# Kernel tuning notes

Measured on AMD Instinct MI355X. Metric: run time of the kernel, lower is better.

Reference implementation:

```python
import jax, jax.numpy as jnp
import numpy as np

N_ATOMS = 40000
N_EDGES = 640000
N_BASIS = 128    # n_atom_basis == n_filters
N_RBF = 20
N_LAYERS = 3
MAX_Z = 100
CUTOFF = 5.0


def _ssp(x):
    # shifted softplus: softplus(x) - log(2)
    return jax.nn.softplus(x) - jnp.log(2.0).astype(x.dtype)


def setup_inputs() -> dict:
    key = jax.random.key(0)
    ks = jax.random.split(key, 16)
    s = 0.05
    inp = {
        'atomic_numbers': jax.random.randint(ks[0], (N_ATOMS,), 0, MAX_Z),
        'r_ij': jax.random.normal(ks[1], (N_EDGES, 3), dtype=jnp.float32),
        'idx_i': jnp.sort(jax.random.randint(ks[2], (N_EDGES,), 0, N_ATOMS)),
        'idx_j': jax.random.randint(ks[3], (N_EDGES,), 0, N_ATOMS),
        # learned parameters (stacked over interaction blocks)
        'emb': jax.random.normal(ks[4], (MAX_Z, N_BASIS), dtype=jnp.float32) * s,
        'in2f_W': jax.random.normal(ks[5], (N_LAYERS, N_BASIS, N_BASIS), dtype=jnp.float32) * s,
        'filt_W1': jax.random.normal(ks[6], (N_LAYERS, N_RBF, N_BASIS), dtype=jnp.float32) * s,
        'filt_b1': jax.random.normal(ks[7], (N_LAYERS, N_BASIS), dtype=jnp.float32) * s,
        'filt_W2': jax.random.normal(ks[8], (N_LAYERS, N_BASIS, N_BASIS), dtype=jnp.float32) * s,
        'filt_b2': jax.random.normal(ks[9], (N_LAYERS, N_BASIS), dtype=jnp.float32) * s,
        'out_W1': jax.random.normal(ks[10], (N_LAYERS, N_BASIS, N_BASIS), dtype=jnp.float32) * s,
        'out_b1': jax.random.normal(ks[11], (N_LAYERS, N_BASIS), dtype=jnp.float32) * s,
        'out_W2': jax.random.normal(ks[12], (N_LAYERS, N_BASIS, N_BASIS), dtype=jnp.float32) * s,
        'out_b2': jax.random.normal(ks[13], (N_LAYERS, N_BASIS), dtype=jnp.float32) * s,
    }
    return inp


def reference(atomic_numbers, r_ij, idx_i, idx_j, emb, in2f_W,
              filt_W1, filt_b1, filt_W2, filt_b2,
              out_W1, out_b1, out_W2, out_b2):
    x = emb[atomic_numbers]                                   # [N, F]
    # pairwise distances and radial basis expansion (GaussianRBF)
    d_ij = jnp.linalg.norm(r_ij, axis=1)                      # [E]
    offsets = jnp.linspace(0.0, CUTOFF, N_RBF, dtype=d_ij.dtype)
    coeff = -0.5 / (offsets[1] - offsets[0]) ** 2
    f_ij = jnp.exp(coeff * (d_ij[:, None] - offsets[None, :]) ** 2)  # [E, n_rbf]
    # cosine cutoff
    rcut_ij = 0.5 * (jnp.cos(d_ij * jnp.pi / CUTOFF) + 1.0) * (d_ij < CUTOFF)
    for l in range(N_LAYERS):
        h = x @ in2f_W[l]                                     # in2f (no bias) [N, F]
        Wij = _ssp(f_ij @ filt_W1[l] + filt_b1[l]) @ filt_W2[l] + filt_b2[l]
        Wij = Wij * rcut_ij[:, None]                          # [E, F]
        msg = h[idx_j] * Wij                                  # gather + filter-multiply
        agg = jax.ops.segment_sum(msg, idx_i, num_segments=N_ATOMS)  # scatter-sum [N, F]
        v = _ssp(agg @ out_W1[l] + out_b1[l]) @ out_W2[l] + out_b2[l]
        x = x + v                                             # residual update
    return x
```

## Files before the change

### kernel.cpp

```cpp
#include <hip/hip_runtime.h>
#include <math.h>

#define N_ATOMS 40000
#define N_EDGES 640000
#define NB      128
#define NRBF    20
#define NLAYERS 3
#define CUTOFF  5.0f
#define DELTA   (CUTOFF / 19.0f)
#define RBF_COEFF (-0.5f / (DELTA * DELTA))
#define LN2F    0.69314718055994531f

#define KTAB    4096
#define TSCALE  ((float)KTAB / CUTOFF)
#define EPB     256
#define EBLKS   (N_EDGES / EPB)
#define TABBLKS 2049

typedef __attribute__((ext_vector_type(8))) short bf16x8;
typedef __attribute__((ext_vector_type(4))) short bf16x4;
typedef __attribute__((ext_vector_type(4))) float fx4;

__device__ __forceinline__ float ssp_f(float x) {
    return fmaxf(x, 0.f) + __logf(1.f + __expf(-fabsf(x))) - LN2F;
}

__device__ __forceinline__ unsigned short bf16_rne(float x) {
    unsigned u = __float_as_uint(x);
    unsigned r = u + 0x7fffu + ((u >> 16) & 1u);
    return (unsigned short)(r >> 16);
}

__device__ __forceinline__ float bfl(unsigned u) { return __uint_as_float(u << 16); }
__device__ __forceinline__ float bfh(unsigned u) { return __uint_as_float(u & 0xffff0000u); }


template<int ZERO>
__device__ __forceinline__ void stage_A_agg(float* __restrict__ A, int row0, int kc,
                                            short* Ah, int tid) {
    #pragma unroll
    for (int it = 0; it < 4; ++it) {
        int idx4 = tid + it * 256;
        int r = idx4 >> 4, kq = (idx4 & 15) << 2;
        float* src = A + (size_t)(row0 + r) * NB + kc * 64 + kq;
        float4 v = *(const float4*)src;
        if (ZERO) *(float4*)src = make_float4(0.f, 0.f, 0.f, 0.f);
        bf16x4 hs;
        const float* vf = (const float*)&v;
        #pragma unroll
        for (int j = 0; j < 4; ++j) hs[j] = (short)bf16_rne(vf[j]);
        int wi = r * 64 + (kq ^ ((r & 7) << 3));
        *(bf16x4*)(Ah + wi) = hs;
    }
}

__device__ __forceinline__ void stage_A_emb(const float* __restrict__ emb,
                                            const int* __restrict__ z, int row0, int kc,
                                            short* Ah, int tid) {
    #pragma unroll
    for (int it = 0; it < 4; ++it) {
        int idx4 = tid + it * 256;
        int r = idx4 >> 4, kq = (idx4 & 15) << 2;
        int zr = z[row0 + r];
        float4 v = *(const float4*)(emb + (size_t)zr * NB + kc * 64 + kq);
        bf16x4 hs;
        const float* vf = (const float*)&v;
        #pragma unroll
        for (int j = 0; j < 4; ++j) hs[j] = (short)bf16_rne(vf[j]);
        int wi = r * 64 + (kq ^ ((r & 7) << 3));
        *(bf16x4*)(Ah + wi) = hs;
    }
}

__device__ __forceinline__ void stage_W(const short* __restrict__ imgh,
                                        short* Wh, int tid) {
    #pragma unroll
    for (int it = 0; it < 4; ++it) {
        int i = tid + it * 256;
        ((bf16x8*)Wh)[i] = ((const bf16x8*)imgh)[i];
    }
}

__device__ __forceinline__ void stage_W_f32(const float* __restrict__ W, int kc,
                                            short* Wh, int tid) {
    #pragma unroll
    for (int it = 0; it < 8; ++it) {
        int i = tid + it * 256;
        int kl = i >> 5;
        int c0 = (i & 31) << 2;
        float4 v = *(const float4*)(W + (size_t)(kc * 64 + kl) * NB + c0);
        const float* vf = (const float*)&v;
        #pragma unroll
        for (int j = 0; j < 4; ++j) {
            int col = c0 + j;
            Wh[col * 64 + (kl ^ ((col & 7) << 3))] = (short)bf16_rne(vf[j]);
        }
    }
}

__device__ __forceinline__ void g_compute(const short* AH, int choff,
                                          const short* Wh,
                                          int wr, int wc, int lane, fx4 acc[2][4]) {
    #pragma unroll
    for (int ks = 0; ks < 2; ++ks) {
        int kb = ks * 32 + (lane >> 4) * 8;
        bf16x8 a_h[2];
        #pragma unroll
        for (int s = 0; s < 2; ++s) {
            int r = wr + s * 16 + (lane & 15);
            int idx = choff + r * 64 + (kb ^ ((r & 7) << 3));
            a_h[s] = *(const bf16x8*)(AH + idx);
        }
        #pragma unroll
        for (int c = 0; c < 4; ++c) {
            int col = wc + c * 16 + (lane & 15);
            int idx = col * 64 + (kb ^ ((col & 7) << 3));
            bf16x8 b_h = *(const bf16x8*)(Wh + idx);
            #pragma unroll
            for (int s = 0; s < 2; ++s)
                acc[s][c] = __builtin_amdgcn_mfma_f32_16x16x32_bf16(a_h[s], b_h, acc[s][c], 0, 0, 0);
        }
    }
}

#define P0_GEMM 625
#define P0_ZERO 1250
#define P0_TAB  TABBLKS
#define P0_DST  625
#define P0_WPR  64
__global__ __launch_bounds__(256) void k_pre0(const int* __restrict__ z,
                                              const float* __restrict__ emb,
                                              const float* __restrict__ r_ij,
                                              const int* __restrict__ ii,
                                              const int* __restrict__ jj,
                                              const float* __restrict__ in2f,
                                              const float* __restrict__ oW1,
                                              const float* __restrict__ oW2,
                                              const float* __restrict__ fW1,
                                              const float* __restrict__ fb1,
                                              const float* __restrict__ fW2,
                                              const float* __restrict__ fb2,
                                              unsigned short* __restrict__ HB,
                                              unsigned short* __restrict__ TabB,
                                              float* __restrict__ AGG,
                                              uint2* __restrict__ PK,
                                              short* __restrict__ Wimg) {
    __shared__ short APOOL[12288];
    int bid = blockIdx.x, tid = threadIdx.x;

    if (bid < P0_GEMM) {
        short* Ah = APOOL;
        short* Wh = APOOL + 4096;
        int wave = tid >> 6, lane = tid & 63;
        int wr = (wave & 1) * 32, wc = (wave >> 1) * 64;
        int row0 = bid * 64;
        fx4 acc[2][4];
        #pragma unroll
        for (int s = 0; s < 2; ++s)
            #pragma unroll
            for (int c = 0; c < 4; ++c)
                acc[s][c] = (fx4){0.f, 0.f, 0.f, 0.f};
        for (int kc = 0; kc < 2; ++kc) {
            if (kc) __syncthreads();
            stage_A_emb(emb, z, row0, kc, Ah, tid);
            stage_W_f32(in2f, kc, Wh, tid);
            __syncthreads();
            g_compute(Ah, 0, Wh, wr, wc, lane, acc);
        }
        #pragma unroll
        for (int s = 0; s < 2; ++s)
            #pragma unroll
            for (int c = 0; c < 4; ++c) {
                int colg = wc + c * 16 + (lane & 15);
                #pragma unroll
                for (int reg = 0; reg < 4; ++reg) {
                    int rowg = row0 + wr + s * 16 + (lane >> 4) * 4 + reg;
                    HB[(size_t)rowg * NB + colg] = bf16_rne(acc[s][c][reg]);
                }
            }
    } else if (bid < P0_GEMM + P0_ZERO) {
        int base = (bid - P0_GEMM) * 4096 + tid * 16;
        float4 zv = make_float4(0.f, 0.f, 0.f, 0.f);
        float4* p = (float4*)(AGG + base);
        p[0] = zv; p[1] = zv; p[2] = zv; p[3] = zv;
    } else if (bid < P0_GEMM + P0_ZERO + P0_TAB) {
        int tb = bid - (P0_GEMM + P0_ZERO);
        int half = tid >> 7, f = tid & 127;
        int r = tb * 2 + half;
        float* tl = (float*)APOOL;
        float val = 0.f;
        float d = (float)r * (CUTOFF / (float)KTAB);
        if (r < KTAB) {
            float a = fb1[f];
            #pragma unroll
            for (int q = 0; q < NRBF; ++q) {
                float dr = d - (float)q * DELTA;
                a += __expf(RBF_COEFF * dr * dr) * fW1[q * NB + f];
            }
            tl[half * NB + f] = ssp_f(a);
        }
        __syncthreads();
        if (r < KTAB) {
            float w = fb2[f];
            #pragma unroll 4
            for (int k = 0; k < NB; ++k) w += tl[half * NB + k] * fW2[k * NB + f];
            float rc = 0.5f * (__cosf(d * ((float)M_PI / CUTOFF)) + 1.f);
            val = w * rc;
        }
        TabB[(size_t)r * NB + f] = bf16_rne(val);
    } else if (bid < P0_GEMM + P0_ZERO + P0_TAB + P0_DST) {
        int e = (bid - (P0_GEMM + P0_ZERO + P0_TAB)) * 1024 + tid * 4;
        const float4* rv = (const float4*)(r_ij + (size_t)e * 3);
        float4 a = rv[0], b = rv[1], c = rv[2];
        int4 iv = *(const int4*)(ii + e);
        int4 jv = *(const int4*)(jj + e);
        float d0 = sqrtf(a.x * a.x + a.y * a.y + a.z * a.z);
        float d1 = sqrtf(a.w * a.w + b.x * b.x + b.y * b.y);
        float d2 = sqrtf(b.z * b.z + b.w * b.w + c.x * c.x);
        float d3 = sqrtf(c.y * c.y + c.z * c.z + c.w * c.w);
        float u0 = fminf(d0 * TSCALE + 0.5f, (float)KTAB);
        float u1 = fminf(d1 * TSCALE + 0.5f, (float)KTAB);
        float u2 = fminf(d2 * TSCALE + 0.5f, (float)KTAB);
        float u3 = fminf(d3 * TSCALE + 0.5f, (float)KTAB);
        uint4 w0, w1;
        w0.x = __float_as_uint(u0); w0.y = ((unsigned)iv.x << 16) | (unsigned)jv.x;
        w0.z = __float_as_uint(u1); w0.w = ((unsigned)iv.y << 16) | (unsigned)jv.y;
        w1.x = __float_as_uint(u2); w1.y = ((unsigned)iv.z << 16) | (unsigned)jv.z;
        w1.z = __float_as_uint(u3); w1.w = ((unsigned)iv.w << 16) | (unsigned)jv.w;
        *(uint4*)(PK + e) = w0;
        *(uint4*)(PK + e + 2) = w1;
    } else {
        int b2 = bid - (P0_GEMM + P0_ZERO + P0_TAB + P0_DST);
        int w = 1 + (b2 >> 3), seg = b2 & 7;
        int layer = w / 3, which = w % 3;
        const float* W = (which == 0 ? in2f : which == 1 ? oW1 : oW2)
                         + (size_t)layer * NB * NB;
        short* hi = Wimg + (size_t)w * 16384;
        int i0 = seg * 2048;
        #pragma unroll
        for (int ofs = 0; ofs < 2048; ofs += 256) {
            int i = i0 + ofs + tid;
            int k = i >> 7, col = i & 127;
            int kc = k >> 6, kl = k & 63;
            hi[kc * 8192 + col * 64 + (kl ^ ((col & 7) << 3))] = (short)bf16_rne(W[i]);
        }
    }
}

__global__ __launch_bounds__(256) void k_edge(const uint2* __restrict__ PK,
                                              const unsigned* __restrict__ HBv,
                                              const unsigned* __restrict__ TabU,
                                              float* __restrict__ AGG,
                                              const float* __restrict__ nW1,
                                              const float* __restrict__ nb1,
                                              const float* __restrict__ nW2,
                                              const float* __restrict__ nb2,
                                              unsigned short* __restrict__ TabN) {
    __shared__ uint2 m_s[EPB];
    __shared__ float t_lds[256];
    int tid = threadIdx.x;
    int bid = blockIdx.x;

    if (bid >= EBLKS) {
        int tb = bid - EBLKS;
        int half = tid >> 7, f = tid & 127;
        int r = tb * 2 + half;
        float val = 0.f;
        float d = (float)r * (CUTOFF / (float)KTAB);
        if (r < KTAB) {
            float a = nb1[f];
            #pragma unroll
            for (int q = 0; q < NRBF; ++q) {
                float dr = d - (float)q * DELTA;
                a += __expf(RBF_COEFF * dr * dr) * nW1[q * NB + f];
            }
            t_lds[half * NB + f] = ssp_f(a);
        }
        __syncthreads();
        if (r < KTAB) {
            float w = nb2[f];
            #pragma unroll 4
            for (int k = 0; k < NB; ++k) w += t_lds[half * NB + k] * nW2[k * NB + f];
            float rc = 0.5f * (__cosf(d * ((float)M_PI / CUTOFF)) + 1.f);
            val = w * rc;
        }
        TabN[(size_t)r * NB + f] = bf16_rne(val);
        return;
    }

    int e0 = bid * EPB;
    m_s[tid] = PK[e0 + tid];
    __syncthreads();

    int wave = tid >> 6, lane = tid & 63;
    int wbase = wave << 6;

    float axA = 0.f, ayA = 0.f, axB = 0.f, ayB = 0.f;
    int curA = -1, curB = -1;
    int nfA = 0, nfB = 0;

    #pragma unroll 4
    for (int t = 0; t < 32; ++t) {
        uint2 mA = m_s[wbase + t];
        uint2 mB = m_s[wbase + 32 + t];

        int kA = (int)__uint_as_float(mA.x);
        int kB = (int)__uint_as_float(mB.x);
        int iaA = (int)(mA.y >> 16), jaA = (int)(mA.y & 0xffffu);
        int iaB = (int)(mB.y >> 16), jaB = (int)(mB.y & 0xffffu);

        unsigned tvA = TabU[kA * 64 + lane];
        unsigned tvB = TabU[kB * 64 + lane];
        unsigned hqA = HBv[jaA * 64 + lane];
        unsigned hqB = HBv[jaB * 64 + lane];

        if (iaA != curA) {
            if (curA >= 0) {
                float* p = AGG + curA * NB + 2 * lane;
                if (nfA == 0) { atomicAdd(p, axA); atomicAdd(p + 1, ayA); }
                else          { *(float2*)p = make_float2(axA, ayA); }
                ++nfA;
            }
            axA = 0.f; ayA = 0.f;
            curA = iaA;
        }
        axA = fmaf(bfl(hqA), bfl(tvA), axA);
        ayA = fmaf(bfh(hqA), bfh(tvA), ayA);

        if (iaB != curB) {
            if (curB >= 0) {
                float* p = AGG + curB * NB + 2 * lane;
                if (nfB == 0) { atomicAdd(p, axB); atomicAdd(p + 1, ayB); }
                else          { *(float2*)p = make_float2(axB, ayB); }
                ++nfB;
            }
            axB = 0.f; ayB = 0.f;
            curB = iaB;
        }
        axB = fmaf(bfl(hqB), bfl(tvB), axB);
        ayB = fmaf(bfh(hqB), bfh(tvB), ayB);
    }
    if (curA >= 0) {
        float* p = AGG + curA * NB + 2 * lane;
        atomicAdd(p, axA); atomicAdd(p + 1, ayA);
    }
    if (curB >= 0) {
        float* p = AGG + curB * NB + 2 * lane;
        atomicAdd(p, axB); atomicAdd(p + 1, ayB);
    }
}

template<int FIRST, int LAST>
__global__ __launch_bounds__(256) void k_fuse(float* __restrict__ AGG,
                                              const short* __restrict__ img1,
                                              const float* __restrict__ b1,
                                              const short* __restrict__ img2,
                                              const float* __restrict__ b2,
                                              const short* __restrict__ img0n,
                                              const int* __restrict__ z,
                                              const float* __restrict__ emb,
                                              float* __restrict__ X,
                                              unsigned short* __restrict__ HB) {
    __shared__ short POOL[16384];
    short* Ah = POOL;
    short* Th = POOL;
    short* Wh = POOL + 8192;

    int tid = threadIdx.x;
    int wave = tid >> 6, lane = tid & 63;
    int wr = (wave & 1) * 32, wc = (wave >> 1) * 64;
    int row0 = blockIdx.x * 64;

    fx4 accT[2][4];
    #pragma unroll
    for (int s = 0; s < 2; ++s)
        #pragma unroll
        for (int c = 0; c < 4; ++c)
            accT[s][c] = (fx4){0.f, 0.f, 0.f, 0.f};
    for (int kc = 0; kc < 2; ++kc) {
        if (kc) __syncthreads();
        stage_A_agg<!LAST>(AGG, row0, kc, Ah, tid);
        stage_W(img1 + kc * 8192, Wh, tid);
        __syncthreads();
        g_compute(Ah, 0, Wh, wr, wc, lane, accT);
    }
    __syncthreads();

    #pragma unroll
    for (int s = 0; s < 2; ++s)
        #pragma unroll
        for (int c = 0; c < 4; ++c) {
            int colg = wc + c * 16 + (lane & 15);
            float bv = b1[colg];
            int kc2 = colg >> 6, kl = colg & 63;
            #pragma unroll
            for (int reg = 0; reg < 4; ++reg) {
                int rl = wr + s * 16 + (lane >> 4) * 4 + reg;
                float t = ssp_f(accT[s][c][reg] + bv);
                Th[kc2 * 4096 + rl * 64 + (kl ^ ((rl & 7) << 3))] = (short)bf16_rne(t);
            }
        }
    stage_W(img2, Wh, tid);
    __syncthreads();

    fx4 accV[2][4];
    #pragma unroll
    for (int s = 0; s < 2; ++s)
        #pragma unroll
        for (int c = 0; c < 4; ++c)
            accV[s][c] = (fx4){0.f, 0.f, 0.f, 0.f};
    g_compute(Th, 0, Wh, wr, wc, lane, accV);
    __syncthreads();
    stage_W(img2 + 8192, Wh, tid);
    __syncthreads();
    g_compute(Th, 4096, Wh, wr, wc, lane, accV);
    __syncthreads();

    #pragma unroll
    for (int s = 0; s < 2; ++s)
        #pragma unroll
        for (int c = 0; c < 4; ++c) {
            int colg = wc + c * 16 + (lane & 15);
            float bv = b2[colg];
            int kc2 = colg >> 6, kl = colg & 63;
            #pragma unroll
            for (int reg = 0; reg < 4; ++reg) {
                int rowg = row0 + wr + s * 16 + (lane >> 4) * 4 + reg;
                size_t o = (size_t)rowg * NB + colg;
                float xo;
                if (FIRST) xo = emb[(size_t)z[rowg] * NB + colg];
                else       xo = X[o];
                float xn = xo + accV[s][c][reg] + bv;
                X[o] = xn;
                if (!LAST) {
                    int rl = wr + s * 16 + (lane >> 4) * 4 + reg;
                    Th[kc2 * 4096 + rl * 64 + (kl ^ ((rl & 7) << 3))] = (short)bf16_rne(xn);
                }
            }
        }
    if (LAST) return;

    stage_W(img0n, Wh, tid);
    __syncthreads();
    fx4 accH[2][4];
    #pragma unroll
    for (int s = 0; s < 2; ++s)
        #pragma unroll
        for (int c = 0; c < 4; ++c)
            accH[s][c] = (fx4){0.f, 0.f, 0.f, 0.f};
    g_compute(Th, 0, Wh, wr, wc, lane, accH);
    __syncthreads();
    stage_W(img0n + 8192, Wh, tid);
    __syncthreads();
    g_compute(Th, 4096, Wh, wr, wc, lane, accH);

    #pragma unroll
    for (int s = 0; s < 2; ++s)
        #pragma unroll
        for (int c = 0; c < 4; ++c) {
            int colg = wc + c * 16 + (lane & 15);
            #pragma unroll
            for (int reg = 0; reg < 4; ++reg) {
                int rowg = row0 + wr + s * 16 + (lane >> 4) * 4 + reg;
                HB[(size_t)rowg * NB + colg] = bf16_rne(accH[s][c][reg]);
            }
        }
}

extern "C" void kernel_launch(void* const* d_in, const int* in_sizes, int n_in,
                              void* d_out, int out_size, void* d_ws, size_t ws_size,
                              hipStream_t stream) {
    const int*   z    = (const int*)  d_in[0];
    const float* rij  = (const float*)d_in[1];
    const int*   ii   = (const int*)  d_in[2];
    const int*   jj   = (const int*)  d_in[3];
    const float* emb  = (const float*)d_in[4];
    const float* in2f = (const float*)d_in[5];
    const float* fW1  = (const float*)d_in[6];
    const float* fb1  = (const float*)d_in[7];
    const float* fW2  = (const float*)d_in[8];
    const float* fb2  = (const float*)d_in[9];
    const float* oW1  = (const float*)d_in[10];
    const float* ob1  = (const float*)d_in[11];
    const float* oW2  = (const float*)d_in[12];
    const float* ob2  = (const float*)d_in[13];

    const int NXF = N_ATOMS * NB;

    float* X = (float*)d_out;
    unsigned short* HB   = (unsigned short*)d_ws;
    float*          AGG  = (float*)(HB + (size_t)NXF);
    uint2*          PK   = (uint2*)(AGG + (size_t)NXF);
    unsigned short* Tab0 = (unsigned short*)(PK + N_EDGES);
    unsigned short* Tab1 = Tab0 + (size_t)4098 * NB;
    short*          Wimg = (short*)(Tab1 + (size_t)4098 * NB);

    k_pre0<<<P0_GEMM + P0_ZERO + P0_TAB + P0_DST + P0_WPR, 256, 0, stream>>>(
        z, emb, rij, ii, jj, in2f, oW1, oW2,
        fW1, fb1, fW2, fb2, HB, Tab0, AGG, PK, Wimg);

    for (int l = 0; l < NLAYERS; ++l) {
        unsigned short* TabCur = (l & 1) ? Tab1 : Tab0;
        unsigned short* TabNxt = (l & 1) ? Tab0 : Tab1;
        int ln = (l < NLAYERS - 1) ? l + 1 : 0;
        int grid_e = EBLKS + ((l < NLAYERS - 1) ? TABBLKS : 0);

        k_edge<<<grid_e, 256, 0, stream>>>(PK,
                                           (const unsigned*)HB,
                                           (const unsigned*)TabCur,
                                           AGG,
                                           fW1 + (size_t)ln * NRBF * NB,
                                           fb1 + (size_t)ln * NB,
                                           fW2 + (size_t)ln * NB * NB,
                                           fb2 + (size_t)ln * NB,
                                           TabNxt);

        const short* img1  = Wimg + (size_t)(l * 3 + 1) * 16384;
        const short* img2  = Wimg + (size_t)(l * 3 + 2) * 16384;
        const short* img0n = Wimg + (size_t)((l + 1 < NLAYERS ? (l + 1) * 3 : 3)) * 16384;

        if (l == 0)
            k_fuse<1, 0><<<N_ATOMS / 64, 256, 0, stream>>>(AGG, img1, ob1 + (size_t)l * NB,
                                                           img2, ob2 + (size_t)l * NB,
                                                           img0n, z, emb, X, HB);
        else if (l < NLAYERS - 1)
            k_fuse<0, 0><<<N_ATOMS / 64, 256, 0, stream>>>(AGG, img1, ob1 + (size_t)l * NB,
                                                           img2, ob2 + (size_t)l * NB,
                                                           img0n, z, emb, X, HB);
        else
            k_fuse<0, 1><<<N_ATOMS / 64, 256, 0, stream>>>(AGG, img1, ob1 + (size_t)l * NB,
                                                           img2, ob2 + (size_t)l * NB,
                                                           img0n, z, emb, X, HB);
    }
}
```

Baseline: 232.9 us.

## Shrink filter table to 128 rows in LDS with linear interpolation

Reduces the precomputed distance-indexed filter table from 4096 nearest-neighbour rows to 128 rows plus a guard row. Each edge block copies the table into shared memory and linearly interpolates between adjacent rows, replacing global table gathers with LDS reads. Edges per block double to 512 to amortise the table load, and the table-build blocks shrink accordingly. The cost is extra interpolation arithmetic and lower accuracy versus the finer table, along with fewer, larger edge blocks.

```diff
diff --git a/kernel.cpp b/kernel.cpp
--- a/kernel.cpp
+++ b/kernel.cpp
@@ -11,11 +11,12 @@
 #define RBF_COEFF (-0.5f / (DELTA * DELTA))
 #define LN2F    0.69314718055994531f
 
-#define KTAB    4096
+#define KTAB    128
+#define TROWS   (KTAB + 2)
 #define TSCALE  ((float)KTAB / CUTOFF)
-#define EPB     256
+#define EPB     512
 #define EBLKS   (N_EDGES / EPB)
-#define TABBLKS 2049
+#define TABBLKS 65
 
 typedef __attribute__((ext_vector_type(8))) short bf16x8;
 typedef __attribute__((ext_vector_type(4))) short bf16x4;
@@ -218,10 +219,10 @@
         float d1 = sqrtf(a.w * a.w + b.x * b.x + b.y * b.y);
         float d2 = sqrtf(b.z * b.z + b.w * b.w + c.x * c.x);
         float d3 = sqrtf(c.y * c.y + c.z * c.z + c.w * c.w);
-        float u0 = fminf(d0 * TSCALE + 0.5f, (float)KTAB);
-        float u1 = fminf(d1 * TSCALE + 0.5f, (float)KTAB);
-        float u2 = fminf(d2 * TSCALE + 0.5f, (float)KTAB);
-        float u3 = fminf(d3 * TSCALE + 0.5f, (float)KTAB);
+        float u0 = fminf(d0 * TSCALE, (float)KTAB);
+        float u1 = fminf(d1 * TSCALE, (float)KTAB);
+        float u2 = fminf(d2 * TSCALE, (float)KTAB);
+        float u3 = fminf(d3 * TSCALE, (float)KTAB);
         uint4 w0, w1;
         w0.x = __float_as_uint(u0); w0.y = ((unsigned)iv.x << 16) | (unsigned)jv.x;
         w0.z = __float_as_uint(u1); w0.w = ((unsigned)iv.y << 16) | (unsigned)jv.y;
@@ -249,15 +250,15 @@
 
 __global__ __launch_bounds__(256) void k_edge(const uint2* __restrict__ PK,
                                               const unsigned* __restrict__ HBv,
-                                              const unsigned* __restrict__ TabU,
+                                              const unsigned* __restrict__ TabG,
                                               float* __restrict__ AGG,
                                               const float* __restrict__ nW1,
                                               const float* __restrict__ nb1,
                                               const float* __restrict__ nW2,
                                               const float* __restrict__ nb2,
                                               unsigned short* __restrict__ TabN) {
+    __shared__ unsigned tab_s[TROWS * 64];
     __shared__ uint2 m_s[EPB];
-    __shared__ float t_lds[256];
     int tid = threadIdx.x;
     int bid = blockIdx.x;
 
@@ -265,6 +266,7 @@
         int tb = bid - EBLKS;
         int half = tid >> 7, f = tid & 127;
         int r = tb * 2 + half;
+        float* tl = (float*)tab_s;
         float val = 0.f;
         float d = (float)r * (CUTOFF / (float)KTAB);
         if (r < KTAB) {
@@ -274,13 +276,13 @@
                 float dr = d - (float)q * DELTA;
                 a += __expf(RBF_COEFF * dr * dr) * nW1[q * NB + f];
             }
-            t_lds[half * NB + f] = ssp_f(a);
+            tl[half * NB + f] = ssp_f(a);
         }
         __syncthreads();
         if (r < KTAB) {
             float w = nb2[f];
             #pragma unroll 4
-            for (int k = 0; k < NB; ++k) w += t_lds[half * NB + k] * nW2[k * NB + f];
+            for (int k = 0; k < NB; ++k) w += tl[half * NB + k] * nW2[k * NB + f];
             float rc = 0.5f * (__cosf(d * ((float)M_PI / CUTOFF)) + 1.f);
             val = w * rc;
         }
@@ -288,31 +290,44 @@
         return;
     }
 
+    for (int i = tid; i < TROWS * 32; i += 256)
+        ((uint2*)tab_s)[i] = ((const uint2*)TabG)[i];
     int e0 = bid * EPB;
-    m_s[tid] = PK[e0 + tid];
+    m_s[tid]       = PK[e0 + tid];
+    m_s[tid + 256] = PK[e0 + 256 + tid];
     __syncthreads();
 
     int wave = tid >> 6, lane = tid & 63;
-    int wbase = wave << 6;
+    int wbase = wave << 7;
 
     float axA = 0.f, ayA = 0.f, axB = 0.f, ayB = 0.f;
     int curA = -1, curB = -1;
     int nfA = 0, nfB = 0;
 
-    #pragma unroll 4
-    for (int t = 0; t < 32; ++t) {
+    #pragma unroll 2
+    for (int t = 0; t < 64; ++t) {
         uint2 mA = m_s[wbase + t];
-        uint2 mB = m_s[wbase + 32 + t];
-
-        int kA = (int)__uint_as_float(mA.x);
-        int kB = (int)__uint_as_float(mB.x);
+        uint2 mB = m_s[wbase + 64 + t];
+
+        float uA = __uint_as_float(mA.x);
+        float uB = __uint_as_float(mB.x);
+        int kA = (int)uA, kB = (int)uB;
+        float frA = uA - (float)kA;
+        float frB = uB - (float)kB;
         int iaA = (int)(mA.y >> 16), jaA = (int)(mA.y & 0xffffu);
         int iaB = (int)(mB.y >> 16), jaB = (int)(mB.y & 0xffffu);
 
-        unsigned tvA = TabU[kA * 64 + lane];
-        unsigned tvB = TabU[kB * 64 + lane];
+        unsigned t0A = tab_s[kA * 64 + lane];
+        unsigned t1A = tab_s[kA * 64 + 64 + lane];
+        unsigned t0B = tab_s[kB * 64 + lane];
+        unsigned t1B = tab_s[kB * 64 + 64 + lane];
         unsigned hqA = HBv[jaA * 64 + lane];
         unsigned hqB = HBv[jaB * 64 + lane];
+
+        float w0A = fmaf(frA, bfl(t1A) - bfl(t0A), bfl(t0A));
+        float w1A = fmaf(frA, bfh(t1A) - bfh(t0A), bfh(t0A));
+        float w0B = fmaf(frB, bfl(t1B) - bfl(t0B), bfl(t0B));
+        float w1B = fmaf(frB, bfh(t1B) - bfh(t0B), bfh(t0B));
 
         if (iaA != curA) {
             if (curA >= 0) {
@@ -324,8 +339,8 @@
             axA = 0.f; ayA = 0.f;
             curA = iaA;
         }
-        axA = fmaf(bfl(hqA), bfl(tvA), axA);
-        ayA = fmaf(bfh(hqA), bfh(tvA), ayA);
+        axA = fmaf(bfl(hqA), w0A, axA);
+        ayA = fmaf(bfh(hqA), w1A, ayA);
 
         if (iaB != curB) {
             if (curB >= 0) {
@@ -337,8 +352,8 @@
             axB = 0.f; ayB = 0.f;
             curB = iaB;
         }
-        axB = fmaf(bfl(hqB), bfl(tvB), axB);
-        ayB = fmaf(bfh(hqB), bfh(tvB), ayB);
+        axB = fmaf(bfl(hqB), w0B, axB);
+        ayB = fmaf(bfh(hqB), w1B, ayB);
     }
     if (curA >= 0) {
         float* p = AGG + curA * NB + 2 * lane;
@@ -492,8 +507,8 @@
     float*          AGG  = (float*)(HB + (size_t)NXF);
     uint2*          PK   = (uint2*)(AGG + (size_t)NXF);
     unsigned short* Tab0 = (unsigned short*)(PK + N_EDGES);
-    unsigned short* Tab1 = Tab0 + (size_t)4098 * NB;
-    short*          Wimg = (short*)(Tab1 + (size_t)4098 * NB);
+    unsigned short* Tab1 = Tab0 + (size_t)TROWS * NB;
+    short*          Wimg = (short*)(Tab1 + (size_t)TROWS * NB);
 
     k_pre0<<<P0_GEMM + P0_ZERO + P0_TAB + P0_DST + P0_WPR, 256, 0, stream>>>(
         z, emb, rij, ii, jj, in2f, oW1, oW2,
```

New measurement: 261.1 us. 12.1% more time.

## Use CSR row pointers for atom-owned segment sums and shrink filter table with interpolation

Applied to the files above, without the earlier changes.

Builds a CSR row-pointer array by binary search over the sorted idx_i, then assigns each wave a fixed range of atoms so segment sums are written with plain stores instead of atomics. This removes the separate AGG zeroing pass and per-layer re-zeroing, and atoms with no edges get explicit zero writes. The filter lookup table shrinks from 4096 to 256 rows and uses linear interpolation between adjacent rows, which costs an extra table load per edge but makes the table much cheaper to build and more cache-resident. Per-wave work now depends on atom degree, so load balance is less even than the fixed edge blocking it replaces.

```diff
diff --git a/kernel.cpp b/kernel.cpp
--- a/kernel.cpp
+++ b/kernel.cpp
@@ -11,11 +11,11 @@
 #define RBF_COEFF (-0.5f / (DELTA * DELTA))
 #define LN2F    0.69314718055994531f
 
-#define KTAB    4096
+#define KTAB    256
+#define TROWS   (KTAB + 2)
 #define TSCALE  ((float)KTAB / CUTOFF)
-#define EPB     256
-#define EBLKS   (N_EDGES / EPB)
-#define TABBLKS 2049
+#define EBLKS   1250
+#define TABBLKS (TROWS / 2)
 
 typedef __attribute__((ext_vector_type(8))) short bf16x8;
 typedef __attribute__((ext_vector_type(4))) short bf16x4;
@@ -35,16 +35,13 @@
 __device__ __forceinline__ float bfh(unsigned u) { return __uint_as_float(u & 0xffff0000u); }
 
 
-template<int ZERO>
-__device__ __forceinline__ void stage_A_agg(float* __restrict__ A, int row0, int kc,
+__device__ __forceinline__ void stage_A_f32(const float* __restrict__ A, int row0, int kc,
                                             short* Ah, int tid) {
     #pragma unroll
     for (int it = 0; it < 4; ++it) {
         int idx4 = tid + it * 256;
         int r = idx4 >> 4, kq = (idx4 & 15) << 2;
-        float* src = A + (size_t)(row0 + r) * NB + kc * 64 + kq;
-        float4 v = *(const float4*)src;
-        if (ZERO) *(float4*)src = make_float4(0.f, 0.f, 0.f, 0.f);
+        float4 v = *(const float4*)(A + (size_t)(row0 + r) * NB + kc * 64 + kq);
         bf16x4 hs;
         const float* vf = (const float*)&v;
         #pragma unroll
@@ -124,10 +121,10 @@
 }
 
 #define P0_GEMM 625
-#define P0_ZERO 1250
 #define P0_TAB  TABBLKS
 #define P0_DST  625
 #define P0_WPR  64
+#define P0_RPT  157
 __global__ __launch_bounds__(256) void k_pre0(const int* __restrict__ z,
                                               const float* __restrict__ emb,
                                               const float* __restrict__ r_ij,
@@ -142,8 +139,8 @@
                                               const float* __restrict__ fb2,
                                               unsigned short* __restrict__ HB,
                                               unsigned short* __restrict__ TabB,
-                                              float* __restrict__ AGG,
                                               uint2* __restrict__ PK,
+                                              int* __restrict__ rp,
                                               short* __restrict__ Wimg) {
     __shared__ short APOOL[12288];
     int bid = blockIdx.x, tid = threadIdx.x;
@@ -178,13 +175,8 @@
                     HB[(size_t)rowg * NB + colg] = bf16_rne(acc[s][c][reg]);
                 }
             }
-    } else if (bid < P0_GEMM + P0_ZERO) {
-        int base = (bid - P0_GEMM) * 4096 + tid * 16;
-        float4 zv = make_float4(0.f, 0.f, 0.f, 0.f);
-        float4* p = (float4*)(AGG + base);
-        p[0] = zv; p[1] = zv; p[2] = zv; p[3] = zv;
-    } else if (bid < P0_GEMM + P0_ZERO + P0_TAB) {
-        int tb = bid - (P0_GEMM + P0_ZERO);
+    } else if (bid < P0_GEMM + P0_TAB) {
+        int tb = bid - P0_GEMM;
         int half = tid >> 7, f = tid & 127;
         int r = tb * 2 + half;
         float* tl = (float*)APOOL;
@@ -208,8 +200,8 @@
             val = w * rc;
         }
         TabB[(size_t)r * NB + f] = bf16_rne(val);
-    } else if (bid < P0_GEMM + P0_ZERO + P0_TAB + P0_DST) {
-        int e = (bid - (P0_GEMM + P0_ZERO + P0_TAB)) * 1024 + tid * 4;
+    } else if (bid < P0_GEMM + P0_TAB + P0_DST) {
+        int e = (bid - (P0_GEMM + P0_TAB)) * 1024 + tid * 4;
         const float4* rv = (const float4*)(r_ij + (size_t)e * 3);
         float4 a = rv[0], b = rv[1], c = rv[2];
         int4 iv = *(const int4*)(ii + e);
@@ -218,10 +210,10 @@
         float d1 = sqrtf(a.w * a.w + b.x * b.x + b.y * b.y);
         float d2 = sqrtf(b.z * b.z + b.w * b.w + c.x * c.x);
         float d3 = sqrtf(c.y * c.y + c.z * c.z + c.w * c.w);
-        float u0 = fminf(d0 * TSCALE + 0.5f, (float)KTAB);
-        float u1 = fminf(d1 * TSCALE + 0.5f, (float)KTAB);
-        float u2 = fminf(d2 * TSCALE + 0.5f, (float)KTAB);
-        float u3 = fminf(d3 * TSCALE + 0.5f, (float)KTAB);
+        float u0 = fminf(d0 * TSCALE, (float)KTAB);
+        float u1 = fminf(d1 * TSCALE, (float)KTAB);
+        float u2 = fminf(d2 * TSCALE, (float)KTAB);
+        float u3 = fminf(d3 * TSCALE, (float)KTAB);
         uint4 w0, w1;
         w0.x = __float_as_uint(u0); w0.y = ((unsigned)iv.x << 16) | (unsigned)jv.x;
         w0.z = __float_as_uint(u1); w0.w = ((unsigned)iv.y << 16) | (unsigned)jv.y;
@@ -229,8 +221,8 @@
         w1.z = __float_as_uint(u3); w1.w = ((unsigned)iv.w << 16) | (unsigned)jv.w;
         *(uint4*)(PK + e) = w0;
         *(uint4*)(PK + e + 2) = w1;
-    } else {
-        int b2 = bid - (P0_GEMM + P0_ZERO + P0_TAB + P0_DST);
+    } else if (bid < P0_GEMM + P0_TAB + P0_DST + P0_WPR) {
+        int b2 = bid - (P0_GEMM + P0_TAB + P0_DST);
         int w = 1 + (b2 >> 3), seg = b2 & 7;
         int layer = w / 3, which = w % 3;
         const float* W = (which == 0 ? in2f : which == 1 ? oW1 : oW2)
@@ -244,10 +236,22 @@
             int kc = k >> 6, kl = k & 63;
             hi[kc * 8192 + col * 64 + (kl ^ ((col & 7) << 3))] = (short)bf16_rne(W[i]);
         }
-    }
-}
-
-__global__ __launch_bounds__(256) void k_edge(const uint2* __restrict__ PK,
+    } else {
+        int a = (bid - (P0_GEMM + P0_TAB + P0_DST + P0_WPR)) * 256 + tid;
+        if (a <= N_ATOMS) {
+            int lo = 0, hi = N_EDGES;
+            #pragma unroll 1
+            while (lo < hi) {
+                int mid = (lo + hi) >> 1;
+                if (ii[mid] < a) lo = mid + 1; else hi = mid;
+            }
+            rp[a] = lo;
+        }
+    }
+}
+
+__global__ __launch_bounds__(256) void k_edge(const int* __restrict__ rp,
+                                              const uint2* __restrict__ PK,
                                               const unsigned* __restrict__ HBv,
                                               const unsigned* __restrict__ TabU,
                                               float* __restrict__ AGG,
@@ -256,7 +260,6 @@
                                               const float* __restrict__ nW2,
                                               const float* __restrict__ nb2,
                                               unsigned short* __restrict__ TabN) {
-    __shared__ uint2 m_s[EPB];
     __shared__ float t_lds[256];
     int tid = threadIdx.x;
     int bid = blockIdx.x;
@@ -288,70 +291,79 @@
         return;
     }
 
-    int e0 = bid * EPB;
-    m_s[tid] = PK[e0 + tid];
-    __syncthreads();
-
     int wave = tid >> 6, lane = tid & 63;
-    int wbase = wave << 6;
+    int A0 = (bid * 4 + wave) * 8;
+    int esA = rp[A0],     eeA = rp[A0 + 4];
+    int esB = rp[A0 + 4], eeB = rp[A0 + 8];
 
     float axA = 0.f, ayA = 0.f, axB = 0.f, ayB = 0.f;
     int curA = -1, curB = -1;
-    int nfA = 0, nfB = 0;
-
-    #pragma unroll 4
-    for (int t = 0; t < 32; ++t) {
-        uint2 mA = m_s[wbase + t];
-        uint2 mB = m_s[wbase + 32 + t];
-
-        int kA = (int)__uint_as_float(mA.x);
-        int kB = (int)__uint_as_float(mB.x);
-        int iaA = (int)(mA.y >> 16), jaA = (int)(mA.y & 0xffffu);
-        int iaB = (int)(mB.y >> 16), jaB = (int)(mB.y & 0xffffu);
-
-        unsigned tvA = TabU[kA * 64 + lane];
-        unsigned tvB = TabU[kB * 64 + lane];
-        unsigned hqA = HBv[jaA * 64 + lane];
-        unsigned hqB = HBv[jaB * 64 + lane];
-
-        if (iaA != curA) {
-            if (curA >= 0) {
-                float* p = AGG + curA * NB + 2 * lane;
-                if (nfA == 0) { atomicAdd(p, axA); atomicAdd(p + 1, ayA); }
-                else          { *(float2*)p = make_float2(axA, ayA); }
-                ++nfA;
-            }
-            axA = 0.f; ayA = 0.f;
-            curA = iaA;
-        }
-        axA = fmaf(bfl(hqA), bfl(tvA), axA);
-        ayA = fmaf(bfh(hqA), bfh(tvA), ayA);
-
-        if (iaB != curB) {
-            if (curB >= 0) {
-                float* p = AGG + curB * NB + 2 * lane;
-                if (nfB == 0) { atomicAdd(p, axB); atomicAdd(p + 1, ayB); }
-                else          { *(float2*)p = make_float2(axB, ayB); }
-                ++nfB;
-            }
-            axB = 0.f; ayB = 0.f;
-            curB = iaB;
-        }
-        axB = fmaf(bfl(hqB), bfl(tvB), axB);
-        ayB = fmaf(bfh(hqB), bfh(tvB), ayB);
-    }
-    if (curA >= 0) {
-        float* p = AGG + curA * NB + 2 * lane;
-        atomicAdd(p, axA); atomicAdd(p + 1, ayA);
-    }
-    if (curB >= 0) {
-        float* p = AGG + curB * NB + 2 * lane;
-        atomicAdd(p, axB); atomicAdd(p + 1, ayB);
-    }
+    int eA = esA, eB = esB;
+
+    while (eA < eeA || eB < eeB) {
+        int nA = min(64, eeA - eA);
+        int nB = min(64, eeB - eB);
+        uint2 mAr = make_uint2(0u, 0u), mBr = make_uint2(0u, 0u);
+        if (nA > 0) mAr = PK[min(eA + lane, eeA - 1)];
+        if (nB > 0) mBr = PK[min(eB + lane, eeB - 1)];
+        int nmax = max(nA, nB);
+        for (int t = 0; t < nmax; ++t) {
+            if (t < nA) {
+                unsigned mx = __shfl(mAr.x, t);
+                unsigned my = __shfl(mAr.y, t);
+                float u = __uint_as_float(mx);
+                int k = (int)u;
+                float fr = u - (float)k;
+                int ia = (int)(my >> 16), ja = (int)(my & 0xffffu);
+                unsigned t0 = TabU[k * 64 + lane];
+                unsigned t1 = TabU[k * 64 + 64 + lane];
+                unsigned hq = HBv[ja * 64 + lane];
+                float w0 = fmaf(fr, bfl(t1) - bfl(t0), bfl(t0));
+                float w1 = fmaf(fr, bfh(t1) - bfh(t0), bfh(t0));
+                if (ia != curA) {
+                    if (curA >= 0)
+                        *(float2*)(AGG + curA * NB + 2 * lane) = make_float2(axA, ayA);
+                    axA = 0.f; ayA = 0.f;
+                    curA = ia;
+                }
+                axA = fmaf(bfl(hq), w0, axA);
+                ayA = fmaf(bfh(hq), w1, ayA);
+            }
+            if (t < nB) {
+                unsigned mx = __shfl(mBr.x, t);
+                unsigned my = __shfl(mBr.y, t);
+                float u = __uint_as_float(mx);
+                int k = (int)u;
+                float fr = u - (float)k;
+                int ia = (int)(my >> 16), ja = (int)(my & 0xffffu);
+                unsigned t0 = TabU[k * 64 + lane];
+                unsigned t1 = TabU[k * 64 + 64 + lane];
+                unsigned hq = HBv[ja * 64 + lane];
+                float w0 = fmaf(fr, bfl(t1) - bfl(t0), bfl(t0));
+                float w1 = fmaf(fr, bfh(t1) - bfh(t0), bfh(t0));
+                if (ia != curB) {
+                    if (curB >= 0)
+                        *(float2*)(AGG + curB * NB + 2 * lane) = make_float2(axB, ayB);
+                    axB = 0.f; ayB = 0.f;
+                    curB = ia;
+                }
+                axB = fmaf(bfl(hq), w0, axB);
+                ayB = fmaf(bfh(hq), w1, ayB);
+            }
+        }
+        eA += nA; eB += nB;
+    }
+    if (curA >= 0) *(float2*)(AGG + curA * NB + 2 * lane) = make_float2(axA, ayA);
+    if (curB >= 0) *(float2*)(AGG + curB * NB + 2 * lane) = make_float2(axB, ayB);
+
+    #pragma unroll
+    for (int a = A0; a < A0 + 8; ++a)
+        if (rp[a] == rp[a + 1])
+            *(float2*)(AGG + a * NB + 2 * lane) = make_float2(0.f, 0.f);
 }
 
 template<int FIRST, int LAST>
-__global__ __launch_bounds__(256) void k_fuse(float* __restrict__ AGG,
+__global__ __launch_bounds__(256) void k_fuse(const float* __restrict__ AGG,
                                               const short* __restrict__ img1,
                                               const float* __restrict__ b1,
                                               const short* __restrict__ img2,
@@ -379,7 +391,7 @@
             accT[s][c] = (fx4){0.f, 0.f, 0.f, 0.f};
     for (int kc = 0; kc < 2; ++kc) {
         if (kc) __syncthreads();
-        stage_A_agg<!LAST>(AGG, row0, kc, Ah, tid);
+        stage_A_f32(AGG, row0, kc, Ah, tid);
         stage_W(img1 + kc * 8192, Wh, tid);
         __syncthreads();
         g_compute(Ah, 0, Wh, wr, wc, lane, accT);
@@ -492,12 +504,13 @@
     float*          AGG  = (float*)(HB + (size_t)NXF);
     uint2*          PK   = (uint2*)(AGG + (size_t)NXF);
     unsigned short* Tab0 = (unsigned short*)(PK + N_EDGES);
-    unsigned short* Tab1 = Tab0 + (size_t)4098 * NB;
-    short*          Wimg = (short*)(Tab1 + (size_t)4098 * NB);
-
-    k_pre0<<<P0_GEMM + P0_ZERO + P0_TAB + P0_DST + P0_WPR, 256, 0, stream>>>(
+    unsigned short* Tab1 = Tab0 + (size_t)TROWS * NB;
+    int*            RP   = (int*)(Tab1 + (size_t)TROWS * NB);
+    short*          Wimg = (short*)(RP + (N_ATOMS + 4));
+
+    k_pre0<<<P0_GEMM + P0_TAB + P0_DST + P0_WPR + P0_RPT, 256, 0, stream>>>(
         z, emb, rij, ii, jj, in2f, oW1, oW2,
-        fW1, fb1, fW2, fb2, HB, Tab0, AGG, PK, Wimg);
+        fW1, fb1, fW2, fb2, HB, Tab0, PK, RP, Wimg);
 
     for (int l = 0; l < NLAYERS; ++l) {
         unsigned short* TabCur = (l & 1) ? Tab1 : Tab0;
@@ -505,7 +518,7 @@
         int ln = (l < NLAYERS - 1) ? l + 1 : 0;
         int grid_e = EBLKS + ((l < NLAYERS - 1) ? TABBLKS : 0);
 
-        k_edge<<<grid_e, 256, 0, stream>>>(PK,
+        k_edge<<<grid_e, 256, 0, stream>>>(RP, PK,
                                            (const unsigned*)HB,
                                            (const unsigned*)TabCur,
                                            AGG,
```

Result: slower. 274.5 us (+17.9%).
